# Performance work log

Measured on AMD Instinct MI355X. Metric: run time of the kernel, lower is better.

The kernel has to match this reference:

```python
import jax, jax.numpy as jnp
import numpy as np

F = 64  # filters per ConvLSTM layer

def hard_sigmoid(x):
    return jnp.clip(0.2 * x + 0.5, 0.0, 1.0)

def conv2d_same(x, w):
    # x: (B,H,W,C), w: (kh,kw,Cin,Cout)
    return jax.lax.conv_general_dilated(x, w, window_strides=(1, 1), padding='SAME',
                                        dimension_numbers=('NHWC', 'HWIO', 'NHWC'))

def convlstm2d(x_seq, Wx, Wh, b):
    # x_seq: (B,T,H,W,Cin) -> (B,T,H,W,F). Keras gate order: i, f, c, o.
    B, T, H, W, _ = x_seq.shape
    h0 = jnp.zeros((B, H, W, F), x_seq.dtype)
    c0 = h0
    def step(carry, x_t):
        h, c = carry
        z = conv2d_same(x_t, Wx) + conv2d_same(h, Wh) + b  # (B,H,W,4F)
        i, f, g, o = jnp.split(z, 4, axis=-1)
        c = hard_sigmoid(f) * c + hard_sigmoid(i) * jnp.tanh(g)
        h = hard_sigmoid(o) * jnp.tanh(c)
        return (h, c), h
    xs = jnp.moveaxis(x_seq, 1, 0)  # time-major
    _, hs = jax.lax.scan(step, (h0, c0), xs)
    return jnp.moveaxis(hs, 0, 1)

def setup_inputs() -> dict:
    key = jax.random.key(0)
    ks = jax.random.split(key, 16)
    B, n_steps, n_feat, n_out = 64, 2048, 64, 1
    s = 0.05
    def rn(k, shape):
        return jax.random.normal(k, shape, dtype=jnp.float32) * s
    inp = {'x': jax.random.normal(ks[0], (B, 1, 1, n_steps, n_feat), dtype=jnp.float32)}
    kernels = [(10, n_feat), (5, F), (10, F), (5, F)]
    for li, (kh, cin) in enumerate(kernels, start=1):
        inp[f'W{li}x'] = rn(ks[3 * li - 2], (kh, 1, cin, 4 * F))
        inp[f'W{li}h'] = rn(ks[3 * li - 1], (kh, 1, F, 4 * F))
        inp[f'b{li}'] = jnp.zeros((4 * F,), jnp.float32)
    flat_dim = 1 * 1 * n_steps * F
    inp['D1w'] = rn(ks[13], (flat_dim, 64))
    inp['D1b'] = jnp.zeros((64,), jnp.float32)
    inp['D2w'] = rn(ks[14], (64, n_out))
    inp['D2b'] = jnp.zeros((n_out,), jnp.float32)
    return inp

def reference(x, W1x, W1h, b1, W2x, W2h, b2, W3x, W3h, b3, W4x, W4h, b4, D1w, D1b, D2w, D2b):
    h = convlstm2d(x, W1x, W1h, b1)   # dropout layers are identity at inference
    h = convlstm2d(h, W2x, W2h, b2)
    h = convlstm2d(h, W3x, W3h, b3)
    h = convlstm2d(h, W4x, W4h, b4)
    flat = h.reshape(h.shape[0], -1)  # (B, T*H*W*F)
    y = jax.nn.relu(flat @ D1w + D1b)
    return y @ D2w + D2b
```

## Files before the change

### kernel.cpp

```cpp
#include <hip/hip_runtime.h>


#define POS 131072
#define SH 80
#define SA 136

typedef __attribute__((ext_vector_type(8))) short bf16x8;
typedef __attribute__((ext_vector_type(4))) float f32x4;

__device__ __forceinline__ unsigned short f2bf_rn(float f) {
    unsigned u = __float_as_uint(f);
    u += 0x7FFF + ((u >> 16) & 1);
    return (unsigned short)(u >> 16);
}
__device__ __forceinline__ float bf2f(unsigned short h) {
    return __uint_as_float(((unsigned)h) << 16);
}
__device__ __forceinline__ float hsig(float x) {
    return fminf(fmaxf(fmaf(x, 0.2f, 0.5f), 0.0f), 1.0f);
}
__device__ __forceinline__ float tanh_e(float x) {
    float t = __expf(2.0f * x);
    return 1.0f - __fdividef(2.0f, t + 1.0f);
}

__global__ __launch_bounds__(256) void prep_w(
    const float* __restrict__ W1, const float* __restrict__ W2,
    const float* __restrict__ W3, const float* __restrict__ W4,
    unsigned short* __restrict__ WT)
{
    const int bid = blockIdx.x;
    const int ll = bid / 3;
    const int g  = bid - ll * 3;
    const float* W = (ll == 0) ? (W1 + 4 * 16384) :
                     (ll == 1) ? (W2 + 2 * 16384) :
                     (ll == 2) ? (W3 + 4 * 16384) : (W4 + 2 * 16384);
    const int gofs = (g == 0) ? 0 : ((g == 1) ? 128 : 192);
    unsigned short* hi = WT + ll * (2 * 192 * 64) + (g * 64) * 64;
    unsigned short* lo = hi + 192 * 64;
    const int n  = threadIdx.x & 63;
    const int c0 = threadIdx.x >> 6;
    #pragma unroll
    for (int cc = 0; cc < 16; cc++) {
        int c = cc * 4 + c0;
        float w = W[c * 256 + gofs + n];
        unsigned short h = f2bf_rn(w);
        hi[n * 64 + c] = h;
        lo[n * 64 + c] = f2bf_rn(w - bf2f(h));
    }
}

__global__ __launch_bounds__(256) void prep_d1(
    const float* __restrict__ D1w,
    unsigned short* __restrict__ Bhig, unsigned short* __restrict__ Blog)
{
    __shared__ unsigned short Thi[64][SA], Tlo[64][SA];
    const int t = threadIdx.x;
    const int k0 = blockIdx.x * 128;
    #pragma unroll
    for (int i = 0; i < 8; i++) {
        int lin4 = t + i * 256;
        int kk = lin4 >> 4;
        int j0 = (lin4 & 15) * 4;
        float4 v = *(const float4*)(D1w + (size_t)(k0 + kk) * 64 + j0);
        const float* vp = (const float*)&v;
        #pragma unroll
        for (int q = 0; q < 4; q++) {
            unsigned short h = f2bf_rn(vp[q]);
            Thi[j0 + q][kk] = h;
            Tlo[j0 + q][kk] = f2bf_rn(vp[q] - bf2f(h));
        }
    }
    __syncthreads();
    #pragma unroll
    for (int i = 0; i < 4; i++) {
        int lin = t + i * 256;
        int nr = lin >> 4;
        int c8 = (lin & 15) * 8;
        size_t g = (size_t)nr * 131072 + k0 + c8;
        *(uint4*)(Bhig + g) = *(const uint4*)&Thi[nr][c8];
        *(uint4*)(Blog + g) = *(const uint4*)&Tlo[nr][c8];
    }
}

__global__ __launch_bounds__(256) void fused_mfma(
    const float* __restrict__ x,
    const unsigned short* __restrict__ WT,
    const float* __restrict__ B1, const float* __restrict__ B2,
    const float* __restrict__ B3, const float* __restrict__ B4,
    unsigned short* __restrict__ h4hi, unsigned short* __restrict__ h4lo)
{
    __shared__ unsigned short Hhi[64][SH];
    __shared__ unsigned short Hlo[64][SH];

    const int t = threadIdx.x;
    const int lane = t & 63;
    const int w = t >> 6;
    const int tx = lane & 15;
    const int quad = lane >> 4;
    const int n = 16 * w + tx;
    const int pbase = blockIdx.x * 64;

    {
        const float4* xv = (const float4*)(x + (size_t)pbase * 64);
        #pragma unroll
        for (int k = 0; k < 4; k++) {
            int lin4 = t + k * 256;
            int p = lin4 >> 4;
            int c0 = (lin4 & 15) * 4;
            float4 v = xv[lin4];
            const float* vp = (const float*)&v;
            unsigned short h0 = f2bf_rn(vp[0]), h1 = f2bf_rn(vp[1]);
            unsigned short h2 = f2bf_rn(vp[2]), h3 = f2bf_rn(vp[3]);
            unsigned hh01 = (unsigned)h0 | ((unsigned)h1 << 16);
            unsigned hh23 = (unsigned)h2 | ((unsigned)h3 << 16);
            unsigned ll01 = (unsigned)f2bf_rn(vp[0] - bf2f(h0)) |
                            ((unsigned)f2bf_rn(vp[1] - bf2f(h1)) << 16);
            unsigned ll23 = (unsigned)f2bf_rn(vp[2] - bf2f(h2)) |
                            ((unsigned)f2bf_rn(vp[3] - bf2f(h3)) << 16);
            *(uint2*)&Hhi[p][c0] = make_uint2(hh01, hh23);
            *(uint2*)&Hlo[p][c0] = make_uint2(ll01, ll23);
        }
    }
    __syncthreads();

    #pragma unroll 1
    for (int l = 0; l < 4; l++) {
        const unsigned short* wl = WT + l * (2 * 192 * 64);
        const float* Bb = (l == 0) ? B1 : (l == 1) ? B2 : (l == 2) ? B3 : B4;
        const float bi = Bb[n];
        const float bg = Bb[128 + n];
        const float bo = Bb[192 + n];

        f32x4 acc[4][3];
        #pragma unroll
        for (int m = 0; m < 4; m++) {
            acc[m][0] = (f32x4){bi, bi, bi, bi};
            acc[m][1] = (f32x4){bg, bg, bg, bg};
            acc[m][2] = (f32x4){bo, bo, bo, bo};
        }

        #pragma unroll
        for (int ks = 0; ks < 2; ks++) {
            bf16x8 Bh[3], Bl[3];
            #pragma unroll
            for (int g = 0; g < 3; g++) {
                const unsigned short* bp = wl + (g * 64 + n) * 64 + ks * 32 + quad * 8;
                Bh[g] = *(const bf16x8*)bp;
                Bl[g] = *(const bf16x8*)(bp + 192 * 64);
            }
            #pragma unroll
            for (int m = 0; m < 4; m++) {
                bf16x8 Ah = *(const bf16x8*)&Hhi[m * 16 + tx][ks * 32 + quad * 8];
                bf16x8 Al = *(const bf16x8*)&Hlo[m * 16 + tx][ks * 32 + quad * 8];
                #pragma unroll
                for (int g = 0; g < 3; g++) {
                    acc[m][g] = __builtin_amdgcn_mfma_f32_16x16x32_bf16(Ah, Bh[g], acc[m][g], 0, 0, 0);
                    acc[m][g] = __builtin_amdgcn_mfma_f32_16x16x32_bf16(Ah, Bl[g], acc[m][g], 0, 0, 0);
                    acc[m][g] = __builtin_amdgcn_mfma_f32_16x16x32_bf16(Al, Bh[g], acc[m][g], 0, 0, 0);
                }
            }
        }

        float hv[4][4];
        #pragma unroll
        for (int m = 0; m < 4; m++)
            #pragma unroll
            for (int r = 0; r < 4; r++) {
                float cs = hsig(acc[m][0][r]) * tanh_e(acc[m][1][r]);
                hv[m][r] = hsig(acc[m][2][r]) * tanh_e(cs);
            }

        __syncthreads();
        #pragma unroll
        for (int m = 0; m < 4; m++)
            #pragma unroll
            for (int r = 0; r < 4; r++) {
                int p = m * 16 + quad * 4 + r;
                unsigned short hh = f2bf_rn(hv[m][r]);
                Hhi[p][n] = hh;
                Hlo[p][n] = f2bf_rn(hv[m][r] - bf2f(hh));
            }
        __syncthreads();
    }

    #pragma unroll
    for (int i = 0; i < 2; i++) {
        int lin8 = t + i * 256;
        int p = lin8 >> 3;
        int c0 = (lin8 & 7) * 8;
        uint4 vh = *(const uint4*)&Hhi[p][c0];
        uint4 vl = *(const uint4*)&Hlo[p][c0];
        size_t g = (size_t)(pbase + p) * 64 + c0;
        *(uint4*)(h4hi + g) = vh;
        *(uint4*)(h4lo + g) = vl;
    }
}

__global__ __launch_bounds__(256) void d1_mfma(
    const unsigned short* __restrict__ Ahig, const unsigned short* __restrict__ Alog,
    const unsigned short* __restrict__ Bhig, const unsigned short* __restrict__ Blog,
    float* __restrict__ part)
{
    __shared__ unsigned short Ahi[64][SA], Alo[64][SA];
    const int t = threadIdx.x;
    const int kb = blockIdx.x;
    const int lane = t & 63, w = t >> 6;
    const int tx = lane & 15, quad = lane >> 4;
    const int n = 16 * w + tx;

    f32x4 acc[4];
    #pragma unroll
    for (int m = 0; m < 4; m++) acc[m] = (f32x4){0.0f, 0.0f, 0.0f, 0.0f};

    #pragma unroll
    for (int sub = 0; sub < 2; sub++) {
        const int k0 = kb * 256 + sub * 128;
        if (sub) __syncthreads();
        #pragma unroll
        for (int i = 0; i < 4; i++) {
            int lin = t + i * 256;
            int row = lin >> 4;
            int c8 = (lin & 15) * 8;
            size_t g = (size_t)row * 131072 + k0 + c8;
            *(uint4*)&Ahi[row][c8] = *(const uint4*)(Ahig + g);
            *(uint4*)&Alo[row][c8] = *(const uint4*)(Alog + g);
        }
        __syncthreads();

        #pragma unroll
        for (int ks = 0; ks < 4; ks++) {
            size_t boff = (size_t)n * 131072 + k0 + ks * 32 + quad * 8;
            bf16x8 Bh = *(const bf16x8*)(Bhig + boff);
            bf16x8 Bl = *(const bf16x8*)(Blog + boff);
            #pragma unroll
            for (int m = 0; m < 4; m++) {
                bf16x8 Ah = *(const bf16x8*)&Ahi[m * 16 + tx][ks * 32 + quad * 8];
                bf16x8 Al = *(const bf16x8*)&Alo[m * 16 + tx][ks * 32 + quad * 8];
                acc[m] = __builtin_amdgcn_mfma_f32_16x16x32_bf16(Ah, Bh, acc[m], 0, 0, 0);
                acc[m] = __builtin_amdgcn_mfma_f32_16x16x32_bf16(Ah, Bl, acc[m], 0, 0, 0);
                acc[m] = __builtin_amdgcn_mfma_f32_16x16x32_bf16(Al, Bh, acc[m], 0, 0, 0);
            }
        }
    }

    float* dst = part + (size_t)kb * 4096;
    #pragma unroll
    for (int m = 0; m < 4; m++)
        #pragma unroll
        for (int r = 0; r < 4; r++)
            dst[(m * 16 + quad * 4 + r) * 64 + n] = acc[m][r];
}

__global__ __launch_bounds__(1024) void d1_reduce(
    const float* __restrict__ part, const float* __restrict__ D1b,
    const float* __restrict__ D2w, const float* __restrict__ D2b,
    float* __restrict__ out)
{
    __shared__ float red[16][64];
    const int b = blockIdx.x;
    const int t = threadIdx.x;
    const int j = t & 63, s = t >> 6;
    float acc = 0.0f;
    #pragma unroll 4
    for (int m = 0; m < 32; m++)
        acc += part[(size_t)(s + 16 * m) * 4096 + b * 64 + j];
    red[s][j] = acc;
    __syncthreads();
    if (t < 64) {
        float v = D1b[t];
        #pragma unroll
        for (int s2 = 0; s2 < 16; s2++) v += red[s2][t];
        v = fmaxf(v, 0.0f) * D2w[t];
        #pragma unroll
        for (int off = 32; off > 0; off >>= 1)
            v += __shfl_down(v, off, 64);
        if (t == 0) out[b] = v + D2b[0];
    }
}

extern "C" void kernel_launch(void* const* d_in, const int* in_sizes, int n_in,
                              void* d_out, int out_size, void* d_ws, size_t ws_size,
                              hipStream_t stream) {
    (void)in_sizes; (void)n_in; (void)out_size; (void)ws_size;
    const float* x   = (const float*)d_in[0];
    const float* W1x = (const float*)d_in[1];
    const float* b1  = (const float*)d_in[3];
    const float* W2x = (const float*)d_in[4];
    const float* b2  = (const float*)d_in[6];
    const float* W3x = (const float*)d_in[7];
    const float* b3  = (const float*)d_in[9];
    const float* W4x = (const float*)d_in[10];
    const float* b4  = (const float*)d_in[12];
    const float* D1w = (const float*)d_in[13];
    const float* D1b = (const float*)d_in[14];
    const float* D2w = (const float*)d_in[15];
    const float* D2b = (const float*)d_in[16];
    float* out = (float*)d_out;

    unsigned short* h4hi = (unsigned short*)d_ws;
    unsigned short* h4lo = h4hi + (size_t)POS * 64;
    float* part = (float*)(h4lo + (size_t)POS * 64);
    unsigned short* WT   = (unsigned short*)(part + (size_t)512 * 4096);
    unsigned short* Bhig = WT + 4 * 2 * 192 * 64;
    unsigned short* Blog = Bhig + (size_t)64 * 131072;

    prep_w<<<dim3(12), dim3(256), 0, stream>>>(W1x, W2x, W3x, W4x, WT);
    prep_d1<<<dim3(1024), dim3(256), 0, stream>>>(D1w, Bhig, Blog);
    fused_mfma<<<dim3(POS / 64), dim3(256), 0, stream>>>(
        x, WT, b1, b2, b3, b4, h4hi, h4lo);
    d1_mfma<<<dim3(512), dim3(256), 0, stream>>>(h4hi, h4lo, Bhig, Blog, part);
    d1_reduce<<<dim3(64), dim3(1024), 0, stream>>>(part, D1b, D2w, D2b, out);
}
```

Measured before the change: 213.5 us.

## Fuse ConvLSTM stack with dense D1 GEMM per timestep block

Each block now owns one timestep across all 64 batch rows instead of 64 consecutive positions. After the four ConvLSTM layers it multiplies the h4 tile held in shared memory directly with its own 64x64 slice of D1w, which it converts to hi/lo bf16 on the fly. This removes the h4 round trip through global memory plus the separate prep_d1 and d1_mfma kernels. The cost is a partial-sum buffer four times larger (2048 partials) that d1_reduce must now sum, and strided x loads across the batch dimension.

New measurement: 211.1 us. Within noise of the previous version (-1.1%).

```diff
diff --git a/kernel.cpp b/kernel.cpp
--- a/kernel.cpp
+++ b/kernel.cpp
@@ -3,7 +3,7 @@
 
 #define POS 131072
 #define SH 80
-#define SA 136
+#define SB 72
 
 typedef __attribute__((ext_vector_type(8))) short bf16x8;
 typedef __attribute__((ext_vector_type(4))) float f32x4;
@@ -50,48 +50,17 @@
     }
 }
 
-__global__ __launch_bounds__(256) void prep_d1(
-    const float* __restrict__ D1w,
-    unsigned short* __restrict__ Bhig, unsigned short* __restrict__ Blog)
-{
-    __shared__ unsigned short Thi[64][SA], Tlo[64][SA];
-    const int t = threadIdx.x;
-    const int k0 = blockIdx.x * 128;
-    #pragma unroll
-    for (int i = 0; i < 8; i++) {
-        int lin4 = t + i * 256;
-        int kk = lin4 >> 4;
-        int j0 = (lin4 & 15) * 4;
-        float4 v = *(const float4*)(D1w + (size_t)(k0 + kk) * 64 + j0);
-        const float* vp = (const float*)&v;
-        #pragma unroll
-        for (int q = 0; q < 4; q++) {
-            unsigned short h = f2bf_rn(vp[q]);
-            Thi[j0 + q][kk] = h;
-            Tlo[j0 + q][kk] = f2bf_rn(vp[q] - bf2f(h));
-        }
-    }
-    __syncthreads();
-    #pragma unroll
-    for (int i = 0; i < 4; i++) {
-        int lin = t + i * 256;
-        int nr = lin >> 4;
-        int c8 = (lin & 15) * 8;
-        size_t g = (size_t)nr * 131072 + k0 + c8;
-        *(uint4*)(Bhig + g) = *(const uint4*)&Thi[nr][c8];
-        *(uint4*)(Blog + g) = *(const uint4*)&Tlo[nr][c8];
-    }
-}
-
-__global__ __launch_bounds__(256) void fused_mfma(
+__global__ __launch_bounds__(256) void mega(
     const float* __restrict__ x,
     const unsigned short* __restrict__ WT,
     const float* __restrict__ B1, const float* __restrict__ B2,
     const float* __restrict__ B3, const float* __restrict__ B4,
-    unsigned short* __restrict__ h4hi, unsigned short* __restrict__ h4lo)
+    const float* __restrict__ D1w, float* __restrict__ part)
 {
     __shared__ unsigned short Hhi[64][SH];
     __shared__ unsigned short Hlo[64][SH];
+    __shared__ unsigned short Bhi[64][SB];
+    __shared__ unsigned short Blo[64][SB];
 
     const int t = threadIdx.x;
     const int lane = t & 63;
@@ -99,16 +68,17 @@
     const int tx = lane & 15;
     const int quad = lane >> 4;
     const int n = 16 * w + tx;
-    const int pbase = blockIdx.x * 64;
+    const int bid = blockIdx.x;
 
     {
-        const float4* xv = (const float4*)(x + (size_t)pbase * 64);
+        const float4* xv = (const float4*)x;
         #pragma unroll
         for (int k = 0; k < 4; k++) {
             int lin4 = t + k * 256;
-            int p = lin4 >> 4;
-            int c0 = (lin4 & 15) * 4;
-            float4 v = xv[lin4];
+            int b = lin4 >> 4;
+            int c4 = lin4 & 15;
+            float4 v = xv[((size_t)b * 2048 + bid) * 16 + c4];
+            int c0 = c4 * 4;
             const float* vp = (const float*)&v;
             unsigned short h0 = f2bf_rn(vp[0]), h1 = f2bf_rn(vp[1]);
             unsigned short h2 = f2bf_rn(vp[2]), h3 = f2bf_rn(vp[3]);
@@ -118,8 +88,8 @@
                             ((unsigned)f2bf_rn(vp[1] - bf2f(h1)) << 16);
             unsigned ll23 = (unsigned)f2bf_rn(vp[2] - bf2f(h2)) |
                             ((unsigned)f2bf_rn(vp[3] - bf2f(h3)) << 16);
-            *(uint2*)&Hhi[p][c0] = make_uint2(hh01, hh23);
-            *(uint2*)&Hlo[p][c0] = make_uint2(ll01, ll23);
+            *(uint2*)&Hhi[b][c0] = make_uint2(hh01, hh23);
+            *(uint2*)&Hlo[b][c0] = make_uint2(ll01, ll23);
         }
     }
     __syncthreads();
@@ -185,71 +155,43 @@
     }
 
     #pragma unroll
-    for (int i = 0; i < 2; i++) {
-        int lin8 = t + i * 256;
-        int p = lin8 >> 3;
-        int c0 = (lin8 & 7) * 8;
-        uint4 vh = *(const uint4*)&Hhi[p][c0];
-        uint4 vl = *(const uint4*)&Hlo[p][c0];
-        size_t g = (size_t)(pbase + p) * 64 + c0;
-        *(uint4*)(h4hi + g) = vh;
-        *(uint4*)(h4lo + g) = vl;
-    }
-}
-
-__global__ __launch_bounds__(256) void d1_mfma(
-    const unsigned short* __restrict__ Ahig, const unsigned short* __restrict__ Alog,
-    const unsigned short* __restrict__ Bhig, const unsigned short* __restrict__ Blog,
-    float* __restrict__ part)
-{
-    __shared__ unsigned short Ahi[64][SA], Alo[64][SA];
-    const int t = threadIdx.x;
-    const int kb = blockIdx.x;
-    const int lane = t & 63, w = t >> 6;
-    const int tx = lane & 15, quad = lane >> 4;
-    const int n = 16 * w + tx;
-
-    f32x4 acc[4];
-    #pragma unroll
-    for (int m = 0; m < 4; m++) acc[m] = (f32x4){0.0f, 0.0f, 0.0f, 0.0f};
-
-    #pragma unroll
-    for (int sub = 0; sub < 2; sub++) {
-        const int k0 = kb * 256 + sub * 128;
-        if (sub) __syncthreads();
-        #pragma unroll
-        for (int i = 0; i < 4; i++) {
-            int lin = t + i * 256;
-            int row = lin >> 4;
-            int c8 = (lin & 15) * 8;
-            size_t g = (size_t)row * 131072 + k0 + c8;
-            *(uint4*)&Ahi[row][c8] = *(const uint4*)(Ahig + g);
-            *(uint4*)&Alo[row][c8] = *(const uint4*)(Alog + g);
-        }
-        __syncthreads();
-
-        #pragma unroll
-        for (int ks = 0; ks < 4; ks++) {
-            size_t boff = (size_t)n * 131072 + k0 + ks * 32 + quad * 8;
-            bf16x8 Bh = *(const bf16x8*)(Bhig + boff);
-            bf16x8 Bl = *(const bf16x8*)(Blog + boff);
-            #pragma unroll
-            for (int m = 0; m < 4; m++) {
-                bf16x8 Ah = *(const bf16x8*)&Ahi[m * 16 + tx][ks * 32 + quad * 8];
-                bf16x8 Al = *(const bf16x8*)&Alo[m * 16 + tx][ks * 32 + quad * 8];
-                acc[m] = __builtin_amdgcn_mfma_f32_16x16x32_bf16(Ah, Bh, acc[m], 0, 0, 0);
-                acc[m] = __builtin_amdgcn_mfma_f32_16x16x32_bf16(Ah, Bl, acc[m], 0, 0, 0);
-                acc[m] = __builtin_amdgcn_mfma_f32_16x16x32_bf16(Al, Bh, acc[m], 0, 0, 0);
-            }
-        }
-    }
-
-    float* dst = part + (size_t)kb * 4096;
+    for (int i = 0; i < 4; i++) {
+        int lin4 = t + i * 256;
+        int c = lin4 >> 4;
+        int j0 = (lin4 & 15) * 4;
+        float4 v = *(const float4*)(D1w + ((size_t)bid * 64 + c) * 64 + j0);
+        const float* vp = (const float*)&v;
+        #pragma unroll
+        for (int q = 0; q < 4; q++) {
+            unsigned short h = f2bf_rn(vp[q]);
+            Bhi[j0 + q][c] = h;
+            Blo[j0 + q][c] = f2bf_rn(vp[q] - bf2f(h));
+        }
+    }
+    __syncthreads();
+
+    f32x4 accd[4];
+    #pragma unroll
+    for (int m = 0; m < 4; m++) accd[m] = (f32x4){0.0f, 0.0f, 0.0f, 0.0f};
+    #pragma unroll
+    for (int ks = 0; ks < 2; ks++) {
+        bf16x8 Bh = *(const bf16x8*)&Bhi[n][ks * 32 + quad * 8];
+        bf16x8 Bl = *(const bf16x8*)&Blo[n][ks * 32 + quad * 8];
+        #pragma unroll
+        for (int m = 0; m < 4; m++) {
+            bf16x8 Ah = *(const bf16x8*)&Hhi[m * 16 + tx][ks * 32 + quad * 8];
+            bf16x8 Al = *(const bf16x8*)&Hlo[m * 16 + tx][ks * 32 + quad * 8];
+            accd[m] = __builtin_amdgcn_mfma_f32_16x16x32_bf16(Ah, Bh, accd[m], 0, 0, 0);
+            accd[m] = __builtin_amdgcn_mfma_f32_16x16x32_bf16(Ah, Bl, accd[m], 0, 0, 0);
+            accd[m] = __builtin_amdgcn_mfma_f32_16x16x32_bf16(Al, Bh, accd[m], 0, 0, 0);
+        }
+    }
+    float* dst = part + (size_t)bid * 4096;
     #pragma unroll
     for (int m = 0; m < 4; m++)
         #pragma unroll
         for (int r = 0; r < 4; r++)
-            dst[(m * 16 + quad * 4 + r) * 64 + n] = acc[m][r];
+            dst[(m * 16 + quad * 4 + r) * 64 + n] = accd[m][r];
 }
 
 __global__ __launch_bounds__(1024) void d1_reduce(
@@ -263,7 +205,7 @@
     const int j = t & 63, s = t >> 6;
     float acc = 0.0f;
     #pragma unroll 4
-    for (int m = 0; m < 32; m++)
+    for (int m = 0; m < 128; m++)
         acc += part[(size_t)(s + 16 * m) * 4096 + b * 64 + j];
     red[s][j] = acc;
     __syncthreads();
@@ -298,17 +240,11 @@
     const float* D2b = (const float*)d_in[16];
     float* out = (float*)d_out;
 
-    unsigned short* h4hi = (unsigned short*)d_ws;
-    unsigned short* h4lo = h4hi + (size_t)POS * 64;
-    float* part = (float*)(h4lo + (size_t)POS * 64);
-    unsigned short* WT   = (unsigned short*)(part + (size_t)512 * 4096);
-    unsigned short* Bhig = WT + 4 * 2 * 192 * 64;
-    unsigned short* Blog = Bhig + (size_t)64 * 131072;
+    float* part = (float*)d_ws;
+    unsigned short* WT = (unsigned short*)(part + (size_t)2048 * 4096);
 
     prep_w<<<dim3(12), dim3(256), 0, stream>>>(W1x, W2x, W3x, W4x, WT);
-    prep_d1<<<dim3(1024), dim3(256), 0, stream>>>(D1w, Bhig, Blog);
-    fused_mfma<<<dim3(POS / 64), dim3(256), 0, stream>>>(
-        x, WT, b1, b2, b3, b4, h4hi, h4lo);
-    d1_mfma<<<dim3(512), dim3(256), 0, stream>>>(h4hi, h4lo, Bhig, Blog, part);
+    mega<<<dim3(2048), dim3(256), 0, stream>>>(
+        x, WT, b1, b2, b3, b4, D1w, part);
     d1_reduce<<<dim3(64), dim3(1024), 0, stream>>>(part, D1b, D2w, D2b, out);
 }
```
